# Kernel optimization log

Measured on AMD Instinct MI355X. Metric: run time of the kernel, lower is better.

Reference implementation:

```python
import jax, jax.numpy as jnp
import numpy as np

B, T, D, H = 2, 2048, 1024, 16
DK = D // H


def setup_inputs() -> dict:
    key = jax.random.key(0)
    ks = jax.random.split(key, 13)
    s = 1.0 / np.sqrt(D)
    return {
        "q": jax.random.normal(ks[0], (B, T, D), jnp.float32),
        "k": jax.random.normal(ks[1], (B, T, D), jnp.float32),
        "v": jax.random.normal(ks[2], (B, T, D), jnp.float32),
        "mask": jax.random.randint(ks[3], (B, T, T), 0, 2, jnp.int32),
        "Wq": jax.random.normal(ks[4], (D, D), jnp.float32) * s,
        "bq": jax.random.normal(ks[5], (D,), jnp.float32) * s,
        "Wk": jax.random.normal(ks[6], (D, D), jnp.float32) * s,
        "bk": jax.random.normal(ks[7], (D,), jnp.float32) * s,
        "Wv": jax.random.normal(ks[8], (D, D), jnp.float32) * s,
        "bv": jax.random.normal(ks[9], (D,), jnp.float32) * s,
        "Wo": jax.random.normal(ks[10], (D, D), jnp.float32) * s,
        "bo": jax.random.normal(ks[11], (D,), jnp.float32) * s,
    }


def reference(q, k, v, mask, Wq, bq, Wk, bk, Wv, bv, Wo, bo):
    # Linear projections (torch Linear: x @ W.T + b), split into heads.
    Q = (q @ Wq.T + bq).reshape(B, T, H, DK).transpose(0, 2, 1, 3)  # [B,H,Tq,dk]
    K = (k @ Wk.T + bk).reshape(B, T, H, DK).transpose(0, 2, 1, 3)
    V = (v @ Wv.T + bv).reshape(B, T, H, DK).transpose(0, 2, 1, 3)
    scores = jnp.einsum("bhqd,bhkd->bhqk", Q, K) / jnp.sqrt(jnp.float32(DK))
    # 3-dim mask path: mask==0 -> -1e9, broadcast over heads.
    scores = jnp.where(mask[:, None, :, :] == 0, jnp.float32(-1e9), scores)
    attn = jax.nn.softmax(scores, axis=-1)
    out = jnp.einsum("bhqk,bhkd->bhqd", attn, V)  # [B,H,Tq,dk]
    out = out.transpose(0, 2, 1, 3).reshape(B, T, D)
    return out @ Wo.T + bo
```

## Files before the change

### kernel.cpp

```cpp
#include <hip/hip_runtime.h>
#include <cstdint>
#include <cstddef>

#define TSEQ 2048
#define DMOD 1024
#define NHEAD 16
#define NBATCH 2
#define MT (NBATCH * TSEQ)
#define LOG2E 1.44269504088896340736f

typedef __attribute__((ext_vector_type(8))) __bf16 bf16x8;
typedef __attribute__((ext_vector_type(4))) float f32x4;
typedef __attribute__((ext_vector_type(8))) unsigned short u16x8;
typedef __attribute__((ext_vector_type(4))) unsigned short u16x4;
typedef __attribute__((ext_vector_type(4))) uint32_t u32x4;

__device__ __forceinline__ unsigned short f2bf(float f) {
  uint32_t u = __builtin_bit_cast(uint32_t, f);
  u += 0x7fffu + ((u >> 16) & 1u);
  return (unsigned short)(u >> 16);
}

__device__ __forceinline__ uint32_t cvt_pk_bf16(float a, float b) {
  uint32_t r;
  asm("v_cvt_pk_bf16_f32 %0, %1, %2" : "=v"(r) : "v"(a), "v"(b));
  return r;
}

__device__ __forceinline__ void gload_lds16(const void* g, const void* l) {
  auto gp = (const __attribute__((address_space(1))) uint32_t*)((uintptr_t)g);
  auto lp = (__attribute__((address_space(3))) uint32_t*)((uintptr_t)l);
  __builtin_amdgcn_global_load_lds(gp, lp, 16, 0, 0);
}

__global__ __launch_bounds__(256) void cvt_wm(const float* __restrict__ w0,
                                              const float* __restrict__ w1,
                                              const float* __restrict__ w2,
                                              const float* __restrict__ w3,
                                              const int* __restrict__ m,
                                              unsigned short* __restrict__ dw,
                                              uint32_t* __restrict__ mx) {
  const int bx = blockIdx.x;
  if (bx < 4096) {
    const size_t idx = ((size_t)bx * 256 + threadIdx.x) * 4;
    const int wsel = (int)(idx >> 20);
    const float* s = wsel == 0 ? w0 : (wsel == 1 ? w1 : (wsel == 2 ? w2 : w3));
    const float4 t = *(const float4*)(s + (idx & 0xFFFFFu));
    u16x4 o;
    o[0] = f2bf(t.x); o[1] = f2bf(t.y); o[2] = f2bf(t.z); o[3] = f2bf(t.w);
    *(u16x4*)(dw + idx) = o;
  } else {
    const size_t W = (size_t)(bx - 4096) * 256 + threadIdx.x;
    const int hi = (int)((W >> 3) & 3), ct = (int)(W & 7);
    const size_t bqkt = W >> 5;
    const int kt = (int)(bqkt & 15);
    const size_t bq = bqkt >> 4;
    const int4 mm = *(const int4*)(m + bq * TSEQ + kt * 128 + ct * 16 + hi * 4);
    const uint32_t o = (mm.x ? 0xFFu : 0u) | (mm.y ? 0xFF00u : 0u) |
                       (mm.z ? 0xFF0000u : 0u) | (mm.w ? 0xFF000000u : 0u);
    mx[W] = o;
  }
}

__device__ __forceinline__ void store_c(unsigned short* C, size_t idx, float v) { C[idx] = f2bf(v); }
__device__ __forceinline__ void store_c(float* C, size_t idx, float v) { C[idx] = v; }

template <typename OT, int MF, bool AF32>
__global__ __launch_bounds__(256) void gemm_bt(const void* __restrict__ A0v,
                                               const void* __restrict__ A1v,
                                               const void* __restrict__ A2v,
                                               const unsigned short* __restrict__ W0,
                                               const unsigned short* __restrict__ W1,
                                               const unsigned short* __restrict__ W2,
                                               const float* __restrict__ b0,
                                               const float* __restrict__ b1,
                                               const float* __restrict__ b2,
                                               OT* __restrict__ C0, OT* __restrict__ C1, OT* __restrict__ C2,
                                               float s0, float s1, float s2) {
  constexpr int BM = MF * 32;
  constexpr int NX = 4096 / BM;
  const int nb = gridDim.x, per = nb >> 3, bid = blockIdx.x;
  const int swz = (bid & 7) * per + (bid >> 3);
  const int z = swz / (NX * 8);
  const int rem = swz % (NX * 8);
  const int m0 = (rem >> 3) * BM, n0 = (rem & 7) * 128;

  const void* Av = z == 0 ? A0v : (z == 1 ? A1v : A2v);
  const unsigned short* Bw = z == 0 ? W0 : (z == 1 ? W1 : W2);
  const float* bias = z == 0 ? b0 : (z == 1 ? b1 : b2);
  OT* C = z == 0 ? C0 : (z == 1 ? C1 : C2);
  const float scale = z == 0 ? s0 : (z == 1 ? s1 : s2);

  __shared__ alignas(16) unsigned short As[2][BM * 32];
  __shared__ alignas(16) unsigned short Bs[2][128 * 32];
  const int tid = threadIdx.x;
  const int wid = tid >> 6;
  const int lane = tid & 63;
  const int lo = lane & 15, hi = lane >> 4;
  const int wr = wid >> 1, wc = wid & 1;
  f32x4 acc[MF][4] = {};

  const int r0 = tid >> 2, c8 = (tid & 3) * 8;
  float4 fa[2][2];

  auto loadA = [&](int k0) {
    if constexpr (AF32) {
#pragma unroll
      for (int i = 0; i < 2; ++i) {
        const int chunk = i * 256 + tid;
        const int row = chunk >> 2, cc = (chunk & 3) * 8;
        const float* p = (const float*)Av + (size_t)(m0 + row) * DMOD + k0 + cc;
        fa[i][0] = *(const float4*)p;
        fa[i][1] = *(const float4*)(p + 4);
      }
    }
  };
  auto writeA = [&](int buf) {
    if constexpr (AF32) {
#pragma unroll
      for (int i = 0; i < 2; ++i) {
        const int chunk = i * 256 + tid;
        u32x4 o;
        o[0] = cvt_pk_bf16(fa[i][0].x, fa[i][0].y);
        o[1] = cvt_pk_bf16(fa[i][0].z, fa[i][0].w);
        o[2] = cvt_pk_bf16(fa[i][1].x, fa[i][1].y);
        o[3] = cvt_pk_bf16(fa[i][1].z, fa[i][1].w);
        *(u32x4*)((char*)As + buf * (BM * 64) + chunk * 16) = o;
      }
    }
  };
  auto stage = [&](int buf, int k0) {
#pragma unroll
    for (int i = 0; i < 2; ++i) {
      const int chunk = i * 256 + tid;
      if constexpr (!AF32) {
        if (i < MF / 2)
          gload_lds16((const unsigned short*)Av + (size_t)(m0 + i * 64 + r0) * DMOD + k0 + c8,
                      (const char*)As + buf * (BM * 64) + chunk * 16);
      }
      gload_lds16(Bw + (size_t)(n0 + i * 64 + r0) * DMOD + k0 + c8,
                  (const char*)Bs + buf * 8192 + chunk * 16);
    }
  };

  loadA(0);
  writeA(0);
  stage(0, 0);
  __syncthreads();

  for (int k0 = 0; k0 < DMOD; k0 += 32) {
    const int cur = (k0 >> 5) & 1;
    const bool more = k0 + 32 < DMOD;
    if (more) { loadA(k0 + 32); stage(cur ^ 1, k0 + 32); }

    bf16x8 af[MF], bfr[4];
#pragma unroll
    for (int m = 0; m < MF; ++m)
      af[m] = *(const bf16x8*)((const char*)As + cur * (BM * 64) +
                               (wr * (MF * 16) + m * 16 + lo) * 64 + hi * 16);
#pragma unroll
    for (int n = 0; n < 4; ++n)
      bfr[n] = *(const bf16x8*)((const char*)Bs + cur * 8192 +
                                (wc * 64 + n * 16 + lo) * 64 + hi * 16);
#pragma unroll
    for (int m = 0; m < MF; ++m)
#pragma unroll
      for (int n = 0; n < 4; ++n)
        acc[m][n] = __builtin_amdgcn_mfma_f32_16x16x32_bf16(af[m], bfr[n], acc[m][n], 0, 0, 0);

    if (more) writeA(cur ^ 1);
    __syncthreads();
  }

#pragma unroll
  for (int n = 0; n < 4; ++n) {
    const int col = n0 + wc * 64 + n * 16 + lo;
    const float bv = bias[col];
#pragma unroll
    for (int m = 0; m < MF; ++m) {
      const int row = m0 + wr * (MF * 16) + m * 16 + hi * 4;
#pragma unroll
      for (int r = 0; r < 4; ++r)
        store_c(C, (size_t)(row + r) * DMOD + col, (acc[m][n][r] + bv) * scale);
    }
  }
}

__global__ __launch_bounds__(256) void transpose_v(const unsigned short* __restrict__ Vp,
                                                   unsigned short* __restrict__ Vt) {
  __shared__ alignas(16) unsigned short tile[64][72];
  const int tid = threadIdx.x;
  const int bt0 = blockIdx.x * 64;
  const int h = blockIdx.y;
  const int b = bt0 >> 11;
  const int t0 = bt0 & (TSEQ - 1);
#pragma unroll
  for (int i = 0; i < 2; ++i) {
    const int chunk = i * 256 + tid;
    const int row = chunk >> 3, c = chunk & 7;
    *(uint4*)((char*)&tile[row][0] + c * 16) =
        *(const uint4*)(Vp + (size_t)(bt0 + row) * DMOD + h * 64 + c * 8);
  }
  __syncthreads();
#pragma unroll
  for (int i = 0; i < 2; ++i) {
    const int chunk = i * 256 + tid;
    const int dk = chunk >> 3, c = chunk & 7;
    u16x8 o;
#pragma unroll
    for (int j = 0; j < 8; ++j) {
      const int x = c * 8 + j;
      const int kl = (x & 32) | ((x & 24) >> 1) | ((x & 4) << 2) | (x & 3);
      o[j] = tile[kl][dk];
    }
    *(u16x8*)(Vt + ((size_t)(b * NHEAD + h) * 64 + dk) * TSEQ + t0 + c * 8) = o;
  }
}

__global__ __launch_bounds__(512, 4) void attn_kernel(const unsigned short* __restrict__ Qp,
                                                      const unsigned short* __restrict__ Kp,
                                                      const unsigned short* __restrict__ Vt,
                                                      const uint32_t* __restrict__ mx,
                                                      unsigned short* __restrict__ AO) {
  __shared__ alignas(16) unsigned short Ks[2][128 * 64];
  __shared__ alignas(16) unsigned short Vs[2][64 * 128];
  const int tid = threadIdx.x;
  const int w = tid >> 6, lane = tid & 63;
  const int lo = lane & 15, hi = lane >> 4;
  const int f = blockIdx.x;
  const int swz = (f & 7) * 64 + (f >> 3);
  const int q0 = (swz & 15) * 128;
  const int h = (swz >> 4) & 15;
  const int b = swz >> 8;

  bf16x8 qf[2];
  {
    const unsigned short* qsrc =
        Qp + (size_t)(b * TSEQ + q0 + w * 16 + lo) * DMOD + h * 64 + hi * 8;
    qf[0] = *(const bf16x8*)qsrc;
    qf[1] = *(const bf16x8*)(qsrc + 32);
  }

  bf16x8 ones;
  {
    u32x4 od;
    od[0] = 0x3F803F80u; od[1] = 0x3F803F80u; od[2] = 0x3F803F80u; od[3] = 0x3F803F80u;
    ones = __builtin_bit_cast(bf16x8, od);
  }

  f32x4 o_acc[4] = {};
  f32x4 l_acc = {};

  const size_t kbase = (size_t)(b * TSEQ) * DMOD + h * 64;
  const size_t vbase = (size_t)(b * NHEAD + h) * 64 * TSEQ;

  const int c0 = tid, c1 = 512 + tid;
  const unsigned short* kp0 = Kp + kbase + (size_t)(c0 >> 3) * DMOD + ((c0 & 7) ^ ((c0 >> 3) & 7)) * 8;
  const unsigned short* kp1 = Kp + kbase + (size_t)(c1 >> 3) * DMOD + ((c1 & 7) ^ ((c1 >> 3) & 7)) * 8;
  const unsigned short* vp0 = Vt + vbase + (size_t)(c0 >> 4) * TSEQ + ((c0 & 15) ^ ((c0 >> 4) & 7)) * 8;
  const unsigned short* vp1 = Vt + vbase + (size_t)(c1 >> 4) * TSEQ + ((c1 & 15) ^ ((c1 >> 4) & 7)) * 8;
  const uint32_t* mp = mx + (size_t)(b * TSEQ + q0 + w * 16 + lo) * 512 + hi * 8;
  const int wb0 = c0 * 16, wb1 = c1 * 16;

  int koffA[8], koffB[8];
#pragma unroll
  for (int ct = 0; ct < 8; ++ct) {
    const int kcol = ct * 16 + lo;
    koffA[ct] = kcol * 128 + ((hi ^ (kcol & 7)) * 16);
    koffB[ct] = kcol * 128 + (((4 + hi) ^ (kcol & 7)) * 16);
  }
  int voff[4][4];
#pragma unroll
  for (int vt = 0; vt < 4; ++vt) {
    const int dk = vt * 16 + lo;
#pragma unroll
    for (int c = 0; c < 4; ++c) voff[vt][c] = dk * 256 + (((c * 4 + hi) ^ (dk & 7)) * 16);
  }

  auto stage = [&](int buf) {
    gload_lds16(kp0, (const char*)Ks[buf] + wb0);
    gload_lds16(kp1, (const char*)Ks[buf] + wb1);
    gload_lds16(vp0, (const char*)Vs[buf] + wb0);
    gload_lds16(vp1, (const char*)Vs[buf] + wb1);
    kp0 += (size_t)128 * DMOD; kp1 += (size_t)128 * DMOD;
    vp0 += 128; vp1 += 128;
  };

  const uint32_t selA = 0x01010000u, selB = 0x03030202u;
  const int NT = TSEQ / 128;

  uint4 mc0 = *(const uint4*)mp, mc1 = *(const uint4*)(mp + 4);
  mp += 32;
  stage(0);
  __syncthreads();

  for (int kt = 0; kt < NT; ++kt) {
    uint4 mn0 = mc0, mn1 = mc1;
    if (kt + 1 < NT) {
      mn0 = *(const uint4*)mp;
      mn1 = *(const uint4*)(mp + 4);
      mp += 32;
      stage((kt + 1) & 1);
    }

    const char* ksb = (const char*)Ks[kt & 1];
    const char* vsb = (const char*)Vs[kt & 1];
    f32x4 s[8];
    __builtin_amdgcn_s_setprio(1);
#pragma unroll
    for (int ct = 0; ct < 8; ++ct) {
      bf16x8 kf0 = *(const bf16x8*)(ksb + koffA[ct]);
      bf16x8 kf1 = *(const bf16x8*)(ksb + koffB[ct]);
      f32x4 zz = {0.f, 0.f, 0.f, 0.f};
      s[ct] = __builtin_amdgcn_mfma_f32_16x16x32_bf16(kf0, qf[0], zz, 0, 0, 0);
      s[ct] = __builtin_amdgcn_mfma_f32_16x16x32_bf16(kf1, qf[1], s[ct], 0, 0, 0);
    }
    __builtin_amdgcn_s_setprio(0);

#pragma unroll
    for (int ct = 0; ct < 8; ++ct) {
      s[ct][0] = __builtin_exp2f(s[ct][0]);
      s[ct][1] = __builtin_exp2f(s[ct][1]);
      s[ct][2] = __builtin_exp2f(s[ct][2]);
      s[ct][3] = __builtin_exp2f(s[ct][3]);
    }

    bf16x8 pf[4];
#pragma unroll
    for (int c = 0; c < 4; ++c) {
      const uint32_t We = c == 0 ? mc0.x : (c == 1 ? mc0.z : (c == 2 ? mc1.x : mc1.z));
      const uint32_t Wo = c == 0 ? mc0.y : (c == 1 ? mc0.w : (c == 2 ? mc1.y : mc1.w));
      u32x4 pd;
      pd[0] = cvt_pk_bf16(s[2 * c][0], s[2 * c][1]) & __builtin_amdgcn_perm(We, We, selA);
      pd[1] = cvt_pk_bf16(s[2 * c][2], s[2 * c][3]) & __builtin_amdgcn_perm(We, We, selB);
      pd[2] = cvt_pk_bf16(s[2 * c + 1][0], s[2 * c + 1][1]) & __builtin_amdgcn_perm(Wo, Wo, selA);
      pd[3] = cvt_pk_bf16(s[2 * c + 1][2], s[2 * c + 1][3]) & __builtin_amdgcn_perm(Wo, Wo, selB);
      pf[c] = __builtin_bit_cast(bf16x8, pd);
    }

    __builtin_amdgcn_s_setprio(1);
#pragma unroll
    for (int vt = 0; vt < 4; ++vt) {
#pragma unroll
      for (int c = 0; c < 4; ++c) {
        bf16x8 vf = *(const bf16x8*)(vsb + voff[vt][c]);
        o_acc[vt] = __builtin_amdgcn_mfma_f32_16x16x32_bf16(pf[c], vf, o_acc[vt], 0, 0, 0);
      }
    }
#pragma unroll
    for (int c = 0; c < 4; ++c)
      l_acc = __builtin_amdgcn_mfma_f32_16x16x32_bf16(pf[c], ones, l_acc, 0, 0, 0);
    __builtin_amdgcn_s_setprio(0);

    __syncthreads();
    mc0 = mn0; mc1 = mn1;
  }

#pragma unroll
  for (int r = 0; r < 4; ++r) {
    const float rl = 1.0f / l_acc[r];
    const size_t orow = (size_t)(b * TSEQ + q0 + w * 16 + hi * 4 + r) * DMOD + h * 64;
#pragma unroll
    for (int vt = 0; vt < 4; ++vt)
      AO[orow + vt * 16 + lo] = f2bf(o_acc[vt][r] * rl);
  }
}

extern "C" void kernel_launch(void* const* d_in, const int* in_sizes, int n_in,
                              void* d_out, int out_size, void* d_ws, size_t ws_size,
                              hipStream_t stream) {
  const float* q  = (const float*)d_in[0];
  const float* k  = (const float*)d_in[1];
  const float* v  = (const float*)d_in[2];
  const int* mask = (const int*)d_in[3];
  const float* Wq = (const float*)d_in[4];
  const float* bq = (const float*)d_in[5];
  const float* Wk = (const float*)d_in[6];
  const float* bk = (const float*)d_in[7];
  const float* Wv = (const float*)d_in[8];
  const float* bv = (const float*)d_in[9];
  const float* Wo = (const float*)d_in[10];
  const float* bo = (const float*)d_in[11];
  float* out = (float*)d_out;

  char* ws = (char*)d_ws;
  const size_t SZ_BT = (size_t)MT * DMOD * 2;

  unsigned short* Qp  = (unsigned short*)(ws + 0);
  unsigned short* Kp  = (unsigned short*)(ws + SZ_BT);
  unsigned short* Vp  = (unsigned short*)(ws + 2 * SZ_BT);
  unsigned short* Vt  = (unsigned short*)(ws + 3 * SZ_BT);
  unsigned short* Wqb = (unsigned short*)(ws + 4 * SZ_BT);
  uint32_t*       mx  = (uint32_t*)(ws + 5 * SZ_BT);
  unsigned short* AO  = Vp;
  unsigned short* Wob = Wqb + 3 * DMOD * DMOD;

  const int nW = DMOD * DMOD;

  cvt_wm<<<dim3(4096 + (NBATCH * TSEQ * 16 * 32) / 256), 256, 0, stream>>>(
      Wq, Wk, Wv, Wo, mask, Wqb, mx);

  const float qs = 0.125f * LOG2E;
  gemm_bt<unsigned short, 4, true><<<dim3(768), 256, 0, stream>>>(
      q, k, v, Wqb, Wqb + nW, Wqb + 2 * nW, bq, bk, bv, Qp, Kp, Vp, qs, 1.0f, 1.0f);

  transpose_v<<<dim3(MT / 64, NHEAD), 256, 0, stream>>>(Vp, Vt);

  attn_kernel<<<dim3(512), 512, 0, stream>>>(Qp, Kp, Vt, mx, AO);

  gemm_bt<float, 2, false><<<dim3(512), 256, 0, stream>>>(
      AO, AO, AO, Wob, Wob, Wob, bo, bo, bo, out, out, out, 1.0f, 1.0f, 1.0f);
}
```

Baseline: 140.3 us.

## Fuse V transpose into QKV projection epilogue and shrink QKV GEMM tile

The separate transpose_v kernel is removed; the QKV GEMM now writes the V projection directly in the permuted, transposed per-head layout that attention expects, using a packed 8-element store per lane. To make the epilogue pack two m-fragments, the QKV GEMM tile is reduced from 128 to 64 rows, doubling the grid to 1536 blocks. This saves a kernel launch and a full round trip of V through memory, but the smaller tile lowers data reuse per block and changes the K and Q write pattern.

After: 144.3 us. 1.03x slower.

```diff
diff --git a/kernel.cpp b/kernel.cpp
--- a/kernel.cpp
+++ b/kernel.cpp
@@ -65,7 +65,7 @@
 __device__ __forceinline__ void store_c(unsigned short* C, size_t idx, float v) { C[idx] = f2bf(v); }
 __device__ __forceinline__ void store_c(float* C, size_t idx, float v) { C[idx] = v; }
 
-template <typename OT, int MF, bool AF32>
+template <typename OT, int MF, bool AF32, bool VT>
 __global__ __launch_bounds__(256) void gemm_bt(const void* __restrict__ A0v,
                                                const void* __restrict__ A1v,
                                                const void* __restrict__ A2v,
@@ -79,6 +79,7 @@
                                                float s0, float s1, float s2) {
   constexpr int BM = MF * 32;
   constexpr int NX = 4096 / BM;
+  constexpr int ACH = MF / 2;
   const int nb = gridDim.x, per = nb >> 3, bid = blockIdx.x;
   const int swz = (bid & 7) * per + (bid >> 3);
   const int z = swz / (NX * 8);
@@ -100,31 +101,30 @@
   const int wr = wid >> 1, wc = wid & 1;
   f32x4 acc[MF][4] = {};
 
-  const int r0 = tid >> 2, c8 = (tid & 3) * 8;
-  float4 fa[2][2];
+  float4 fa[ACH][2];
 
   auto loadA = [&](int k0) {
     if constexpr (AF32) {
 #pragma unroll
-      for (int i = 0; i < 2; ++i) {
-        const int chunk = i * 256 + tid;
+      for (int j = 0; j < ACH; ++j) {
+        const int chunk = j * 256 + tid;
         const int row = chunk >> 2, cc = (chunk & 3) * 8;
         const float* p = (const float*)Av + (size_t)(m0 + row) * DMOD + k0 + cc;
-        fa[i][0] = *(const float4*)p;
-        fa[i][1] = *(const float4*)(p + 4);
+        fa[j][0] = *(const float4*)p;
+        fa[j][1] = *(const float4*)(p + 4);
       }
     }
   };
   auto writeA = [&](int buf) {
     if constexpr (AF32) {
 #pragma unroll
-      for (int i = 0; i < 2; ++i) {
-        const int chunk = i * 256 + tid;
+      for (int j = 0; j < ACH; ++j) {
+        const int chunk = j * 256 + tid;
         u32x4 o;
-        o[0] = cvt_pk_bf16(fa[i][0].x, fa[i][0].y);
-        o[1] = cvt_pk_bf16(fa[i][0].z, fa[i][0].w);
-        o[2] = cvt_pk_bf16(fa[i][1].x, fa[i][1].y);
-        o[3] = cvt_pk_bf16(fa[i][1].z, fa[i][1].w);
+        o[0] = cvt_pk_bf16(fa[j][0].x, fa[j][0].y);
+        o[1] = cvt_pk_bf16(fa[j][0].z, fa[j][0].w);
+        o[2] = cvt_pk_bf16(fa[j][1].x, fa[j][1].y);
+        o[3] = cvt_pk_bf16(fa[j][1].z, fa[j][1].w);
         *(u32x4*)((char*)As + buf * (BM * 64) + chunk * 16) = o;
       }
     }
@@ -133,12 +133,13 @@
 #pragma unroll
     for (int i = 0; i < 2; ++i) {
       const int chunk = i * 256 + tid;
+      const int row = chunk >> 2, c8 = (chunk & 3) * 8;
       if constexpr (!AF32) {
-        if (i < MF / 2)
-          gload_lds16((const unsigned short*)Av + (size_t)(m0 + i * 64 + r0) * DMOD + k0 + c8,
+        if (i < ACH)
+          gload_lds16((const unsigned short*)Av + (size_t)(m0 + row) * DMOD + k0 + c8,
                       (const char*)As + buf * (BM * 64) + chunk * 16);
       }
-      gload_lds16(Bw + (size_t)(n0 + i * 64 + r0) * DMOD + k0 + c8,
+      gload_lds16(Bw + (size_t)(n0 + row) * DMOD + k0 + c8,
                   (const char*)Bs + buf * 8192 + chunk * 16);
     }
   };
@@ -172,48 +173,39 @@
     __syncthreads();
   }
 
-#pragma unroll
-  for (int n = 0; n < 4; ++n) {
-    const int col = n0 + wc * 64 + n * 16 + lo;
-    const float bv = bias[col];
-#pragma unroll
-    for (int m = 0; m < MF; ++m) {
-      const int row = m0 + wr * (MF * 16) + m * 16 + hi * 4;
-#pragma unroll
-      for (int r = 0; r < 4; ++r)
-        store_c(C, (size_t)(row + r) * DMOD + col, (acc[m][n][r] + bv) * scale);
-    }
-  }
-}
-
-__global__ __launch_bounds__(256) void transpose_v(const unsigned short* __restrict__ Vp,
-                                                   unsigned short* __restrict__ Vt) {
-  __shared__ alignas(16) unsigned short tile[64][72];
-  const int tid = threadIdx.x;
-  const int bt0 = blockIdx.x * 64;
-  const int h = blockIdx.y;
-  const int b = bt0 >> 11;
-  const int t0 = bt0 & (TSEQ - 1);
-#pragma unroll
-  for (int i = 0; i < 2; ++i) {
-    const int chunk = i * 256 + tid;
-    const int row = chunk >> 3, c = chunk & 7;
-    *(uint4*)((char*)&tile[row][0] + c * 16) =
-        *(const uint4*)(Vp + (size_t)(bt0 + row) * DMOD + h * 64 + c * 8);
-  }
-  __syncthreads();
-#pragma unroll
-  for (int i = 0; i < 2; ++i) {
-    const int chunk = i * 256 + tid;
-    const int dk = chunk >> 3, c = chunk & 7;
-    u16x8 o;
-#pragma unroll
-    for (int j = 0; j < 8; ++j) {
-      const int x = c * 8 + j;
-      const int kl = (x & 32) | ((x & 24) >> 1) | ((x & 4) << 2) | (x & 3);
-      o[j] = tile[kl][dk];
-    }
-    *(u16x8*)(Vt + ((size_t)(b * NHEAD + h) * 64 + dk) * TSEQ + t0 + c * 8) = o;
+  if (VT && z == 2) {
+    static_assert(MF == 2 || !VT, "VT path packs m=0,1");
+    const int tb = m0 + wr * 32 + hi * 4;
+    const int bb = tb >> 11;
+    const int tl = tb & 2047;
+    const int x = (tl & ~63) | (tl & 35) | (((tl >> 2) & 1) << 3) | (((tl >> 3) & 1) << 4);
+#pragma unroll
+    for (int n = 0; n < 4; ++n) {
+      const int dkc = n0 + wc * 64 + n * 16 + lo;
+      const float bv = bias[dkc];
+      const int hh = dkc >> 6, dk = dkc & 63;
+      u16x8 o;
+#pragma unroll
+      for (int m = 0; m < 2; ++m)
+#pragma unroll
+        for (int r = 0; r < 4; ++r)
+          o[m * 4 + r] = f2bf((acc[m][n][r] + bv) * scale);
+      *(u16x8*)((unsigned short*)C +
+                (size_t)((bb * NHEAD + hh) * 64 + dk) * TSEQ + x) = o;
+    }
+  } else {
+#pragma unroll
+    for (int n = 0; n < 4; ++n) {
+      const int col = n0 + wc * 64 + n * 16 + lo;
+      const float bv = bias[col];
+#pragma unroll
+      for (int m = 0; m < MF; ++m) {
+        const int row = m0 + wr * (MF * 16) + m * 16 + hi * 4;
+#pragma unroll
+        for (int r = 0; r < 4; ++r)
+          store_c(C, (size_t)(row + r) * DMOD + col, (acc[m][n][r] + bv) * scale);
+      }
+    }
   }
 }
 
@@ -388,11 +380,10 @@
 
   unsigned short* Qp  = (unsigned short*)(ws + 0);
   unsigned short* Kp  = (unsigned short*)(ws + SZ_BT);
-  unsigned short* Vp  = (unsigned short*)(ws + 2 * SZ_BT);
-  unsigned short* Vt  = (unsigned short*)(ws + 3 * SZ_BT);
+  unsigned short* Vt  = (unsigned short*)(ws + 2 * SZ_BT);
+  unsigned short* AO  = (unsigned short*)(ws + 3 * SZ_BT);
   unsigned short* Wqb = (unsigned short*)(ws + 4 * SZ_BT);
   uint32_t*       mx  = (uint32_t*)(ws + 5 * SZ_BT);
-  unsigned short* AO  = Vp;
   unsigned short* Wob = Wqb + 3 * DMOD * DMOD;
 
   const int nW = DMOD * DMOD;
@@ -401,13 +392,11 @@
       Wq, Wk, Wv, Wo, mask, Wqb, mx);
 
   const float qs = 0.125f * LOG2E;
-  gemm_bt<unsigned short, 4, true><<<dim3(768), 256, 0, stream>>>(
-      q, k, v, Wqb, Wqb + nW, Wqb + 2 * nW, bq, bk, bv, Qp, Kp, Vp, qs, 1.0f, 1.0f);
-
-  transpose_v<<<dim3(MT / 64, NHEAD), 256, 0, stream>>>(Vp, Vt);
+  gemm_bt<unsigned short, 2, true, true><<<dim3(1536), 256, 0, stream>>>(
+      q, k, v, Wqb, Wqb + nW, Wqb + 2 * nW, bq, bk, bv, Qp, Kp, Vt, qs, 1.0f, 1.0f);
 
   attn_kernel<<<dim3(512), 512, 0, stream>>>(Qp, Kp, Vt, mx, AO);
 
-  gemm_bt<float, 2, false><<<dim3(512), 256, 0, stream>>>(
+  gemm_bt<float, 2, false, false><<<dim3(512), 256, 0, stream>>>(
       AO, AO, AO, Wob, Wob, Wob, bo, bo, bo, out, out, out, 1.0f, 1.0f, 1.0f);
 }
```

## Halve attention block threads, each wave computes two 16-row query tiles

Applied to the files above, without the earlier changes.

The attention kernel now launches 256 threads per block instead of 512, with each wave handling 32 query rows as two 16-row groups. Each K and V fragment read from shared memory feeds two MFMAs, which halves LDS read traffic per unit of compute. The cost is higher register pressure from the doubled accumulators and score arrays, and fewer waves available to hide latency. The GEMM A/B staging indexing was also rewritten, and AO now gets its own workspace slot instead of aliasing Vp.

After: 141.7 us. Within noise of the previous version (+1.0%).

```diff
diff --git a/kernel.cpp b/kernel.cpp
--- a/kernel.cpp
+++ b/kernel.cpp
@@ -79,6 +79,7 @@
                                                float s0, float s1, float s2) {
   constexpr int BM = MF * 32;
   constexpr int NX = 4096 / BM;
+  constexpr int ACH = MF / 2;
   const int nb = gridDim.x, per = nb >> 3, bid = blockIdx.x;
   const int swz = (bid & 7) * per + (bid >> 3);
   const int z = swz / (NX * 8);
@@ -100,31 +101,30 @@
   const int wr = wid >> 1, wc = wid & 1;
   f32x4 acc[MF][4] = {};
 
-  const int r0 = tid >> 2, c8 = (tid & 3) * 8;
-  float4 fa[2][2];
+  float4 fa[ACH][2];
 
   auto loadA = [&](int k0) {
     if constexpr (AF32) {
 #pragma unroll
-      for (int i = 0; i < 2; ++i) {
-        const int chunk = i * 256 + tid;
+      for (int j = 0; j < ACH; ++j) {
+        const int chunk = j * 256 + tid;
         const int row = chunk >> 2, cc = (chunk & 3) * 8;
         const float* p = (const float*)Av + (size_t)(m0 + row) * DMOD + k0 + cc;
-        fa[i][0] = *(const float4*)p;
-        fa[i][1] = *(const float4*)(p + 4);
+        fa[j][0] = *(const float4*)p;
+        fa[j][1] = *(const float4*)(p + 4);
       }
     }
   };
   auto writeA = [&](int buf) {
     if constexpr (AF32) {
 #pragma unroll
-      for (int i = 0; i < 2; ++i) {
-        const int chunk = i * 256 + tid;
+      for (int j = 0; j < ACH; ++j) {
+        const int chunk = j * 256 + tid;
         u32x4 o;
-        o[0] = cvt_pk_bf16(fa[i][0].x, fa[i][0].y);
-        o[1] = cvt_pk_bf16(fa[i][0].z, fa[i][0].w);
-        o[2] = cvt_pk_bf16(fa[i][1].x, fa[i][1].y);
-        o[3] = cvt_pk_bf16(fa[i][1].z, fa[i][1].w);
+        o[0] = cvt_pk_bf16(fa[j][0].x, fa[j][0].y);
+        o[1] = cvt_pk_bf16(fa[j][0].z, fa[j][0].w);
+        o[2] = cvt_pk_bf16(fa[j][1].x, fa[j][1].y);
+        o[3] = cvt_pk_bf16(fa[j][1].z, fa[j][1].w);
         *(u32x4*)((char*)As + buf * (BM * 64) + chunk * 16) = o;
       }
     }
@@ -133,12 +133,13 @@
 #pragma unroll
     for (int i = 0; i < 2; ++i) {
       const int chunk = i * 256 + tid;
+      const int row = chunk >> 2, c8 = (chunk & 3) * 8;
       if constexpr (!AF32) {
-        if (i < MF / 2)
-          gload_lds16((const unsigned short*)Av + (size_t)(m0 + i * 64 + r0) * DMOD + k0 + c8,
+        if (i < ACH)
+          gload_lds16((const unsigned short*)Av + (size_t)(m0 + row) * DMOD + k0 + c8,
                       (const char*)As + buf * (BM * 64) + chunk * 16);
       }
-      gload_lds16(Bw + (size_t)(n0 + i * 64 + r0) * DMOD + k0 + c8,
+      gload_lds16(Bw + (size_t)(n0 + row) * DMOD + k0 + c8,
                   (const char*)Bs + buf * 8192 + chunk * 16);
     }
   };
@@ -217,11 +218,11 @@
   }
 }
 
-__global__ __launch_bounds__(512, 4) void attn_kernel(const unsigned short* __restrict__ Qp,
-                                                      const unsigned short* __restrict__ Kp,
-                                                      const unsigned short* __restrict__ Vt,
-                                                      const uint32_t* __restrict__ mx,
-                                                      unsigned short* __restrict__ AO) {
+__global__ __launch_bounds__(256) void attn_kernel(const unsigned short* __restrict__ Qp,
+                                                   const unsigned short* __restrict__ Kp,
+                                                   const unsigned short* __restrict__ Vt,
+                                                   const uint32_t* __restrict__ mx,
+                                                   unsigned short* __restrict__ AO) {
   __shared__ alignas(16) unsigned short Ks[2][128 * 64];
   __shared__ alignas(16) unsigned short Vs[2][64 * 128];
   const int tid = threadIdx.x;
@@ -233,12 +234,15 @@
   const int h = (swz >> 4) & 15;
   const int b = swz >> 8;
 
-  bf16x8 qf[2];
+  bf16x8 qf0[2], qf1[2];
   {
-    const unsigned short* qsrc =
-        Qp + (size_t)(b * TSEQ + q0 + w * 16 + lo) * DMOD + h * 64 + hi * 8;
-    qf[0] = *(const bf16x8*)qsrc;
-    qf[1] = *(const bf16x8*)(qsrc + 32);
+    const unsigned short* qs0 =
+        Qp + (size_t)(b * TSEQ + q0 + w * 32 + lo) * DMOD + h * 64 + hi * 8;
+    qf0[0] = *(const bf16x8*)qs0;
+    qf0[1] = *(const bf16x8*)(qs0 + 32);
+    const unsigned short* qs1 = qs0 + (size_t)16 * DMOD;
+    qf1[0] = *(const bf16x8*)qs1;
+    qf1[1] = *(const bf16x8*)(qs1 + 32);
   }
 
   bf16x8 ones;
@@ -248,19 +252,24 @@
     ones = __builtin_bit_cast(bf16x8, od);
   }
 
-  f32x4 o_acc[4] = {};
-  f32x4 l_acc = {};
+  f32x4 o_acc[2][4] = {};
+  f32x4 l_acc[2] = {};
 
   const size_t kbase = (size_t)(b * TSEQ) * DMOD + h * 64;
   const size_t vbase = (size_t)(b * NHEAD + h) * 64 * TSEQ;
 
-  const int c0 = tid, c1 = 512 + tid;
-  const unsigned short* kp0 = Kp + kbase + (size_t)(c0 >> 3) * DMOD + ((c0 & 7) ^ ((c0 >> 3) & 7)) * 8;
-  const unsigned short* kp1 = Kp + kbase + (size_t)(c1 >> 3) * DMOD + ((c1 & 7) ^ ((c1 >> 3) & 7)) * 8;
-  const unsigned short* vp0 = Vt + vbase + (size_t)(c0 >> 4) * TSEQ + ((c0 & 15) ^ ((c0 >> 4) & 7)) * 8;
-  const unsigned short* vp1 = Vt + vbase + (size_t)(c1 >> 4) * TSEQ + ((c1 & 15) ^ ((c1 >> 4) & 7)) * 8;
-  const uint32_t* mp = mx + (size_t)(b * TSEQ + q0 + w * 16 + lo) * 512 + hi * 8;
-  const int wb0 = c0 * 16, wb1 = c1 * 16;
+  const unsigned short* kp[4];
+  const unsigned short* vp[4];
+  int wb[4];
+#pragma unroll
+  for (int i = 0; i < 4; ++i) {
+    const int c = i * 256 + tid;
+    kp[i] = Kp + kbase + (size_t)(c >> 3) * DMOD + ((c & 7) ^ ((c >> 3) & 7)) * 8;
+    vp[i] = Vt + vbase + (size_t)(c >> 4) * TSEQ + ((c & 15) ^ ((c >> 4) & 7)) * 8;
+    wb[i] = c * 16;
+  }
+  const uint32_t* mp0 = mx + (size_t)(b * TSEQ + q0 + w * 32 + lo) * 512 + hi * 8;
+  const uint32_t* mp1 = mp0 + 16 * 512;
 
   int koffA[8], koffB[8];
 #pragma unroll
@@ -278,64 +287,77 @@
   }
 
   auto stage = [&](int buf) {
-    gload_lds16(kp0, (const char*)Ks[buf] + wb0);
-    gload_lds16(kp1, (const char*)Ks[buf] + wb1);
-    gload_lds16(vp0, (const char*)Vs[buf] + wb0);
-    gload_lds16(vp1, (const char*)Vs[buf] + wb1);
-    kp0 += (size_t)128 * DMOD; kp1 += (size_t)128 * DMOD;
-    vp0 += 128; vp1 += 128;
+#pragma unroll
+    for (int i = 0; i < 4; ++i) {
+      gload_lds16(kp[i], (const char*)Ks[buf] + wb[i]);
+      gload_lds16(vp[i], (const char*)Vs[buf] + wb[i]);
+      kp[i] += (size_t)128 * DMOD;
+      vp[i] += 128;
+    }
   };
 
   const uint32_t selA = 0x01010000u, selB = 0x03030202u;
   const int NT = TSEQ / 128;
 
-  uint4 mc0 = *(const uint4*)mp, mc1 = *(const uint4*)(mp + 4);
-  mp += 32;
+  uint4 ma0 = *(const uint4*)mp0, ma1 = *(const uint4*)(mp0 + 4);
+  uint4 mb0 = *(const uint4*)mp1, mb1 = *(const uint4*)(mp1 + 4);
+  mp0 += 32; mp1 += 32;
   stage(0);
   __syncthreads();
 
   for (int kt = 0; kt < NT; ++kt) {
-    uint4 mn0 = mc0, mn1 = mc1;
+    uint4 na0 = ma0, na1 = ma1, nb0 = mb0, nb1 = mb1;
     if (kt + 1 < NT) {
-      mn0 = *(const uint4*)mp;
-      mn1 = *(const uint4*)(mp + 4);
-      mp += 32;
+      na0 = *(const uint4*)mp0; na1 = *(const uint4*)(mp0 + 4);
+      nb0 = *(const uint4*)mp1; nb1 = *(const uint4*)(mp1 + 4);
+      mp0 += 32; mp1 += 32;
       stage((kt + 1) & 1);
     }
 
     const char* ksb = (const char*)Ks[kt & 1];
     const char* vsb = (const char*)Vs[kt & 1];
-    f32x4 s[8];
+    f32x4 s0[8], s1[8];
     __builtin_amdgcn_s_setprio(1);
 #pragma unroll
     for (int ct = 0; ct < 8; ++ct) {
       bf16x8 kf0 = *(const bf16x8*)(ksb + koffA[ct]);
       bf16x8 kf1 = *(const bf16x8*)(ksb + koffB[ct]);
       f32x4 zz = {0.f, 0.f, 0.f, 0.f};
-      s[ct] = __builtin_amdgcn_mfma_f32_16x16x32_bf16(kf0, qf[0], zz, 0, 0, 0);
-      s[ct] = __builtin_amdgcn_mfma_f32_16x16x32_bf16(kf1, qf[1], s[ct], 0, 0, 0);
+      s0[ct] = __builtin_amdgcn_mfma_f32_16x16x32_bf16(kf0, qf0[0], zz, 0, 0, 0);
+      s1[ct] = __builtin_amdgcn_mfma_f32_16x16x32_bf16(kf0, qf1[0], zz, 0, 0, 0);
+      s0[ct] = __builtin_amdgcn_mfma_f32_16x16x32_bf16(kf1, qf0[1], s0[ct], 0, 0, 0);
+      s1[ct] = __builtin_amdgcn_mfma_f32_16x16x32_bf16(kf1, qf1[1], s1[ct], 0, 0, 0);
     }
     __builtin_amdgcn_s_setprio(0);
 
 #pragma unroll
     for (int ct = 0; ct < 8; ++ct) {
-      s[ct][0] = __builtin_exp2f(s[ct][0]);
-      s[ct][1] = __builtin_exp2f(s[ct][1]);
-      s[ct][2] = __builtin_exp2f(s[ct][2]);
-      s[ct][3] = __builtin_exp2f(s[ct][3]);
-    }
-
-    bf16x8 pf[4];
+#pragma unroll
+      for (int r = 0; r < 4; ++r) {
+        s0[ct][r] = __builtin_exp2f(s0[ct][r]);
+        s1[ct][r] = __builtin_exp2f(s1[ct][r]);
+      }
+    }
+
+    bf16x8 pf0[4], pf1[4];
 #pragma unroll
     for (int c = 0; c < 4; ++c) {
-      const uint32_t We = c == 0 ? mc0.x : (c == 1 ? mc0.z : (c == 2 ? mc1.x : mc1.z));
-      const uint32_t Wo = c == 0 ? mc0.y : (c == 1 ? mc0.w : (c == 2 ? mc1.y : mc1.w));
+      const uint32_t We0 = c == 0 ? ma0.x : (c == 1 ? ma0.z : (c == 2 ? ma1.x : ma1.z));
+      const uint32_t Wo0 = c == 0 ? ma0.y : (c == 1 ? ma0.w : (c == 2 ? ma1.y : ma1.w));
+      const uint32_t We1 = c == 0 ? mb0.x : (c == 1 ? mb0.z : (c == 2 ? mb1.x : mb1.z));
+      const uint32_t Wo1 = c == 0 ? mb0.y : (c == 1 ? mb0.w : (c == 2 ? mb1.y : mb1.w));
       u32x4 pd;
-      pd[0] = cvt_pk_bf16(s[2 * c][0], s[2 * c][1]) & __builtin_amdgcn_perm(We, We, selA);
-      pd[1] = cvt_pk_bf16(s[2 * c][2], s[2 * c][3]) & __builtin_amdgcn_perm(We, We, selB);
-      pd[2] = cvt_pk_bf16(s[2 * c + 1][0], s[2 * c + 1][1]) & __builtin_amdgcn_perm(Wo, Wo, selA);
-      pd[3] = cvt_pk_bf16(s[2 * c + 1][2], s[2 * c + 1][3]) & __builtin_amdgcn_perm(Wo, Wo, selB);
-      pf[c] = __builtin_bit_cast(bf16x8, pd);
+      pd[0] = cvt_pk_bf16(s0[2 * c][0], s0[2 * c][1]) & __builtin_amdgcn_perm(We0, We0, selA);
+      pd[1] = cvt_pk_bf16(s0[2 * c][2], s0[2 * c][3]) & __builtin_amdgcn_perm(We0, We0, selB);
+      pd[2] = cvt_pk_bf16(s0[2 * c + 1][0], s0[2 * c + 1][1]) & __builtin_amdgcn_perm(Wo0, Wo0, selA);
+      pd[3] = cvt_pk_bf16(s0[2 * c + 1][2], s0[2 * c + 1][3]) & __builtin_amdgcn_perm(Wo0, Wo0, selB);
+      pf0[c] = __builtin_bit_cast(bf16x8, pd);
+      u32x4 pe;
+      pe[0] = cvt_pk_bf16(s1[2 * c][0], s1[2 * c][1]) & __builtin_amdgcn_perm(We1, We1, selA);
+      pe[1] = cvt_pk_bf16(s1[2 * c][2], s1[2 * c][3]) & __builtin_amdgcn_perm(We1, We1, selB);
+      pe[2] = cvt_pk_bf16(s1[2 * c + 1][0], s1[2 * c + 1][1]) & __builtin_amdgcn_perm(Wo1, Wo1, selA);
+      pe[3] = cvt_pk_bf16(s1[2 * c + 1][2], s1[2 * c + 1][3]) & __builtin_amdgcn_perm(Wo1, Wo1, selB);
+      pf1[c] = __builtin_bit_cast(bf16x8, pe);
     }
 
     __builtin_amdgcn_s_setprio(1);
@@ -344,25 +366,32 @@
 #pragma unroll
       for (int c = 0; c < 4; ++c) {
         bf16x8 vf = *(const bf16x8*)(vsb + voff[vt][c]);
-        o_acc[vt] = __builtin_amdgcn_mfma_f32_16x16x32_bf16(pf[c], vf, o_acc[vt], 0, 0, 0);
+        o_acc[0][vt] = __builtin_amdgcn_mfma_f32_16x16x32_bf16(pf0[c], vf, o_acc[0][vt], 0, 0, 0);
+        o_acc[1][vt] = __builtin_amdgcn_mfma_f32_16x16x32_bf16(pf1[c], vf, o_acc[1][vt], 0, 0, 0);
       }
     }
 #pragma unroll
-    for (int c = 0; c < 4; ++c)
-      l_acc = __builtin_amdgcn_mfma_f32_16x16x32_bf16(pf[c], ones, l_acc, 0, 0, 0);
+    for (int c = 0; c < 4; ++c) {
+      l_acc[0] = __builtin_amdgcn_mfma_f32_16x16x32_bf16(pf0[c], ones, l_acc[0], 0, 0, 0);
+      l_acc[1] = __builtin_amdgcn_mfma_f32_16x16x32_bf16(pf1[c], ones, l_acc[1], 0, 0, 0);
+    }
     __builtin_amdgcn_s_setprio(0);
 
     __syncthreads();
-    mc0 = mn0; mc1 = mn1;
-  }
-
-#pragma unroll
-  for (int r = 0; r < 4; ++r) {
-    const float rl = 1.0f / l_acc[r];
-    const size_t orow = (size_t)(b * TSEQ + q0 + w * 16 + hi * 4 + r) * DMOD + h * 64;
-#pragma unroll
-    for (int vt = 0; vt < 4; ++vt)
-      AO[orow + vt * 16 + lo] = f2bf(o_acc[vt][r] * rl);
+    ma0 = na0; ma1 = na1; mb0 = nb0; mb1 = nb1;
+  }
+
+#pragma unroll
+  for (int g = 0; g < 2; ++g) {
+#pragma unroll
+    for (int r = 0; r < 4; ++r) {
+      const float rl = 1.0f / l_acc[g][r];
+      const size_t orow =
+          (size_t)(b * TSEQ + q0 + w * 32 + g * 16 + hi * 4 + r) * DMOD + h * 64;
+#pragma unroll
+      for (int vt = 0; vt < 4; ++vt)
+        AO[orow + vt * 16 + lo] = f2bf(o_acc[g][vt][r] * rl);
+    }
   }
 }
 
@@ -390,9 +419,9 @@
   unsigned short* Kp  = (unsigned short*)(ws + SZ_BT);
   unsigned short* Vp  = (unsigned short*)(ws + 2 * SZ_BT);
   unsigned short* Vt  = (unsigned short*)(ws + 3 * SZ_BT);
-  unsigned short* Wqb = (unsigned short*)(ws + 4 * SZ_BT);
-  uint32_t*       mx  = (uint32_t*)(ws + 5 * SZ_BT);
-  unsigned short* AO  = Vp;
+  unsigned short* AO  = (unsigned short*)(ws + 4 * SZ_BT);
+  unsigned short* Wqb = (unsigned short*)(ws + 5 * SZ_BT);
+  uint32_t*       mx  = (uint32_t*)(ws + 6 * SZ_BT);
   unsigned short* Wob = Wqb + 3 * DMOD * DMOD;
 
   const int nW = DMOD * DMOD;
@@ -406,7 +435,7 @@
 
   transpose_v<<<dim3(MT / 64, NHEAD), 256, 0, stream>>>(Vp, Vt);
 
-  attn_kernel<<<dim3(512), 512, 0, stream>>>(Qp, Kp, Vt, mx, AO);
+  attn_kernel<<<dim3(512), 256, 0, stream>>>(Qp, Kp, Vt, mx, AO);
 
   gemm_bt<float, 2, false><<<dim3(512), 256, 0, stream>>>(
       AO, AO, AO, Wob, Wob, Wob, bo, bo, bo, out, out, out, 1.0f, 1.0f, 1.0f);
```

## Fuse fp32 weight conversion into GEMM B-operand loads, drop weight-convert pass

Applied to the files above, without the earlier changes.

Removes the separate pass that converted all four fp32 weight matrices to bf16 in workspace. The GEMMs now load fp32 weights directly into registers and convert them to bf16 while writing LDS, with a launch-bounds occupancy hint added. The mask expansion stays as a standalone kernel. This saves a kernel and about 12 MB of traffic, but each GEMM tile now re-reads weights as fp32 (twice the bytes) and spends more VALU work and registers on conversion, losing the async global-to-LDS path for B.

New measurement: 158.6 us. 1.13x slower.

```diff
diff --git a/kernel.cpp b/kernel.cpp
--- a/kernel.cpp
+++ b/kernel.cpp
@@ -33,52 +33,37 @@
   __builtin_amdgcn_global_load_lds(gp, lp, 16, 0, 0);
 }
 
-__global__ __launch_bounds__(256) void cvt_wm(const float* __restrict__ w0,
-                                              const float* __restrict__ w1,
-                                              const float* __restrict__ w2,
-                                              const float* __restrict__ w3,
-                                              const int* __restrict__ m,
-                                              unsigned short* __restrict__ dw,
-                                              uint32_t* __restrict__ mx) {
-  const int bx = blockIdx.x;
-  if (bx < 4096) {
-    const size_t idx = ((size_t)bx * 256 + threadIdx.x) * 4;
-    const int wsel = (int)(idx >> 20);
-    const float* s = wsel == 0 ? w0 : (wsel == 1 ? w1 : (wsel == 2 ? w2 : w3));
-    const float4 t = *(const float4*)(s + (idx & 0xFFFFFu));
-    u16x4 o;
-    o[0] = f2bf(t.x); o[1] = f2bf(t.y); o[2] = f2bf(t.z); o[3] = f2bf(t.w);
-    *(u16x4*)(dw + idx) = o;
-  } else {
-    const size_t W = (size_t)(bx - 4096) * 256 + threadIdx.x;
-    const int hi = (int)((W >> 3) & 3), ct = (int)(W & 7);
-    const size_t bqkt = W >> 5;
-    const int kt = (int)(bqkt & 15);
-    const size_t bq = bqkt >> 4;
-    const int4 mm = *(const int4*)(m + bq * TSEQ + kt * 128 + ct * 16 + hi * 4);
-    const uint32_t o = (mm.x ? 0xFFu : 0u) | (mm.y ? 0xFF00u : 0u) |
-                       (mm.z ? 0xFF0000u : 0u) | (mm.w ? 0xFF000000u : 0u);
-    mx[W] = o;
-  }
+__global__ __launch_bounds__(256) void mask_exp(const int* __restrict__ m,
+                                                uint32_t* __restrict__ mx) {
+  const size_t W = (size_t)blockIdx.x * 256 + threadIdx.x;
+  const int hi = (int)((W >> 3) & 3), ct = (int)(W & 7);
+  const size_t bqkt = W >> 5;
+  const int kt = (int)(bqkt & 15);
+  const size_t bq = bqkt >> 4;
+  const int4 mm = *(const int4*)(m + bq * TSEQ + kt * 128 + ct * 16 + hi * 4);
+  const uint32_t o = (mm.x ? 0xFFu : 0u) | (mm.y ? 0xFF00u : 0u) |
+                     (mm.z ? 0xFF0000u : 0u) | (mm.w ? 0xFF000000u : 0u);
+  mx[W] = o;
 }
 
 __device__ __forceinline__ void store_c(unsigned short* C, size_t idx, float v) { C[idx] = f2bf(v); }
 __device__ __forceinline__ void store_c(float* C, size_t idx, float v) { C[idx] = v; }
 
 template <typename OT, int MF, bool AF32>
-__global__ __launch_bounds__(256) void gemm_bt(const void* __restrict__ A0v,
-                                               const void* __restrict__ A1v,
-                                               const void* __restrict__ A2v,
-                                               const unsigned short* __restrict__ W0,
-                                               const unsigned short* __restrict__ W1,
-                                               const unsigned short* __restrict__ W2,
-                                               const float* __restrict__ b0,
-                                               const float* __restrict__ b1,
-                                               const float* __restrict__ b2,
-                                               OT* __restrict__ C0, OT* __restrict__ C1, OT* __restrict__ C2,
-                                               float s0, float s1, float s2) {
+__global__ __launch_bounds__(256, 4) void gemm_bt(const void* __restrict__ A0v,
+                                                  const void* __restrict__ A1v,
+                                                  const void* __restrict__ A2v,
+                                                  const float* __restrict__ W0,
+                                                  const float* __restrict__ W1,
+                                                  const float* __restrict__ W2,
+                                                  const float* __restrict__ b0,
+                                                  const float* __restrict__ b1,
+                                                  const float* __restrict__ b2,
+                                                  OT* __restrict__ C0, OT* __restrict__ C1, OT* __restrict__ C2,
+                                                  float s0, float s1, float s2) {
   constexpr int BM = MF * 32;
   constexpr int NX = 4096 / BM;
+  constexpr int ACH = MF / 2;
   const int nb = gridDim.x, per = nb >> 3, bid = blockIdx.x;
   const int swz = (bid & 7) * per + (bid >> 3);
   const int z = swz / (NX * 8);
@@ -86,7 +71,7 @@
   const int m0 = (rem >> 3) * BM, n0 = (rem & 7) * 128;
 
   const void* Av = z == 0 ? A0v : (z == 1 ? A1v : A2v);
-  const unsigned short* Bw = z == 0 ? W0 : (z == 1 ? W1 : W2);
+  const float* Bw = z == 0 ? W0 : (z == 1 ? W1 : W2);
   const float* bias = z == 0 ? b0 : (z == 1 ? b1 : b2);
   OT* C = z == 0 ? C0 : (z == 1 ? C1 : C2);
   const float scale = z == 0 ? s0 : (z == 1 ? s1 : s2);
@@ -100,58 +85,80 @@
   const int wr = wid >> 1, wc = wid & 1;
   f32x4 acc[MF][4] = {};
 
-  const int r0 = tid >> 2, c8 = (tid & 3) * 8;
-  float4 fa[2][2];
+  float4 fa[ACH][2];
+  float4 fb[2][2];
 
   auto loadA = [&](int k0) {
     if constexpr (AF32) {
 #pragma unroll
-      for (int i = 0; i < 2; ++i) {
-        const int chunk = i * 256 + tid;
+      for (int j = 0; j < ACH; ++j) {
+        const int chunk = j * 256 + tid;
         const int row = chunk >> 2, cc = (chunk & 3) * 8;
         const float* p = (const float*)Av + (size_t)(m0 + row) * DMOD + k0 + cc;
-        fa[i][0] = *(const float4*)p;
-        fa[i][1] = *(const float4*)(p + 4);
+        fa[j][0] = *(const float4*)p;
+        fa[j][1] = *(const float4*)(p + 4);
       }
+    }
+  };
+  auto loadB = [&](int k0) {
+#pragma unroll
+    for (int j = 0; j < 2; ++j) {
+      const int chunk = j * 256 + tid;
+      const int row = chunk >> 2, cc = (chunk & 3) * 8;
+      const float* p = Bw + (size_t)(n0 + row) * DMOD + k0 + cc;
+      fb[j][0] = *(const float4*)p;
+      fb[j][1] = *(const float4*)(p + 4);
     }
   };
   auto writeA = [&](int buf) {
     if constexpr (AF32) {
 #pragma unroll
-      for (int i = 0; i < 2; ++i) {
-        const int chunk = i * 256 + tid;
+      for (int j = 0; j < ACH; ++j) {
+        const int chunk = j * 256 + tid;
         u32x4 o;
-        o[0] = cvt_pk_bf16(fa[i][0].x, fa[i][0].y);
-        o[1] = cvt_pk_bf16(fa[i][0].z, fa[i][0].w);
-        o[2] = cvt_pk_bf16(fa[i][1].x, fa[i][1].y);
-        o[3] = cvt_pk_bf16(fa[i][1].z, fa[i][1].w);
+        o[0] = cvt_pk_bf16(fa[j][0].x, fa[j][0].y);
+        o[1] = cvt_pk_bf16(fa[j][0].z, fa[j][0].w);
+        o[2] = cvt_pk_bf16(fa[j][1].x, fa[j][1].y);
+        o[3] = cvt_pk_bf16(fa[j][1].z, fa[j][1].w);
         *(u32x4*)((char*)As + buf * (BM * 64) + chunk * 16) = o;
       }
     }
   };
-  auto stage = [&](int buf, int k0) {
-#pragma unroll
-    for (int i = 0; i < 2; ++i) {
-      const int chunk = i * 256 + tid;
-      if constexpr (!AF32) {
-        if (i < MF / 2)
-          gload_lds16((const unsigned short*)Av + (size_t)(m0 + i * 64 + r0) * DMOD + k0 + c8,
-                      (const char*)As + buf * (BM * 64) + chunk * 16);
+  auto writeB = [&](int buf) {
+#pragma unroll
+    for (int j = 0; j < 2; ++j) {
+      const int chunk = j * 256 + tid;
+      u32x4 o;
+      o[0] = cvt_pk_bf16(fb[j][0].x, fb[j][0].y);
+      o[1] = cvt_pk_bf16(fb[j][0].z, fb[j][0].w);
+      o[2] = cvt_pk_bf16(fb[j][1].x, fb[j][1].y);
+      o[3] = cvt_pk_bf16(fb[j][1].z, fb[j][1].w);
+      *(u32x4*)((char*)Bs + buf * 8192 + chunk * 16) = o;
+    }
+  };
+  auto stageA = [&](int buf, int k0) {
+    if constexpr (!AF32) {
+#pragma unroll
+      for (int i = 0; i < ACH; ++i) {
+        const int chunk = i * 256 + tid;
+        const int row = chunk >> 2, c8 = (chunk & 3) * 8;
+        gload_lds16((const unsigned short*)Av + (size_t)(m0 + row) * DMOD + k0 + c8,
+                    (const char*)As + buf * (BM * 64) + chunk * 16);
       }
-      gload_lds16(Bw + (size_t)(n0 + i * 64 + r0) * DMOD + k0 + c8,
-                  (const char*)Bs + buf * 8192 + chunk * 16);
     }
   };
 
   loadA(0);
+  loadB(0);
   writeA(0);
-  stage(0, 0);
+  writeB(0);
+  stageA(0, 0);
   __syncthreads();
 
   for (int k0 = 0; k0 < DMOD; k0 += 32) {
     const int cur = (k0 >> 5) & 1;
     const bool more = k0 + 32 < DMOD;
-    if (more) { loadA(k0 + 32); stage(cur ^ 1, k0 + 32); }
+    if (more) { loadA(k0 + 32); loadB(k0 + 32); stageA(cur ^ 1, k0 + 32); }
 
     bf16x8 af[MF], bfr[4];
 #pragma unroll
@@ -168,7 +175,7 @@
       for (int n = 0; n < 4; ++n)
         acc[m][n] = __builtin_amdgcn_mfma_f32_16x16x32_bf16(af[m], bfr[n], acc[m][n], 0, 0, 0);
 
-    if (more) writeA(cur ^ 1);
+    if (more) { writeA(cur ^ 1); writeB(cur ^ 1); }
     __syncthreads();
   }
 
@@ -390,24 +397,19 @@
   unsigned short* Kp  = (unsigned short*)(ws + SZ_BT);
   unsigned short* Vp  = (unsigned short*)(ws + 2 * SZ_BT);
   unsigned short* Vt  = (unsigned short*)(ws + 3 * SZ_BT);
-  unsigned short* Wqb = (unsigned short*)(ws + 4 * SZ_BT);
+  unsigned short* AO  = (unsigned short*)(ws + 4 * SZ_BT);
   uint32_t*       mx  = (uint32_t*)(ws + 5 * SZ_BT);
-  unsigned short* AO  = Vp;
-  unsigned short* Wob = Wqb + 3 * DMOD * DMOD;
-
-  const int nW = DMOD * DMOD;
-
-  cvt_wm<<<dim3(4096 + (NBATCH * TSEQ * 16 * 32) / 256), 256, 0, stream>>>(
-      Wq, Wk, Wv, Wo, mask, Wqb, mx);
+
+  mask_exp<<<dim3((NBATCH * TSEQ * 16 * 32) / 256), 256, 0, stream>>>(mask, mx);
 
   const float qs = 0.125f * LOG2E;
   gemm_bt<unsigned short, 4, true><<<dim3(768), 256, 0, stream>>>(
-      q, k, v, Wqb, Wqb + nW, Wqb + 2 * nW, bq, bk, bv, Qp, Kp, Vp, qs, 1.0f, 1.0f);
+      q, k, v, Wq, Wk, Wv, bq, bk, bv, Qp, Kp, Vp, qs, 1.0f, 1.0f);
 
   transpose_v<<<dim3(MT / 64, NHEAD), 256, 0, stream>>>(Vp, Vt);
 
   attn_kernel<<<dim3(512), 512, 0, stream>>>(Qp, Kp, Vt, mx, AO);
 
   gemm_bt<float, 2, false><<<dim3(512), 256, 0, stream>>>(
-      AO, AO, AO, Wob, Wob, Wob, bo, bo, bo, out, out, out, 1.0f, 1.0f, 1.0f);
-}
+      AO, AO, AO, Wo, Wo, Wo, bo, bo, bo, out, out, out, 1.0f, 1.0f, 1.0f);
+}
```
